# Kernel optimization log

Hardware: AMD Instinct MI355X
Metric: run time of the kernel (lower is better)

The kernel has to match this reference:

```python
import jax, jax.numpy as jnp
import numpy as np

D = 128      # embedding_dim
E = 50000    # positive edges per metapath
S = 16       # negative samples per edge
N_A = 100000 # nodes of type A (head type of both metapaths)
N_B = 50000  # nodes of type B (tail type of metapath 1)


def setup_inputs() -> dict:
    key = jax.random.key(0)
    ks = jax.random.split(key, 10)
    emb_A = jax.random.normal(ks[0], (N_A, D), dtype=jnp.float32)
    emb_B = jax.random.normal(ks[1], (N_B, D), dtype=jnp.float32)
    # nn.init.uniform_(a=-1, b=1)
    rel_emb = jax.random.uniform(ks[2], (2, D, D), dtype=jnp.float32, minval=-1.0, maxval=1.0)
    edge_index_m0 = jax.random.randint(ks[3], (2, E), 0, N_A)  # A -> A
    edge_index_m1 = jnp.stack([
        jax.random.randint(ks[4], (E,), 0, N_A),               # heads: type A
        jax.random.randint(ks[5], (E,), 0, N_B),               # tails: type B
    ])
    neg_head_m0 = jax.random.randint(ks[6], (E, S), 0, N_A)
    neg_head_m1 = jax.random.randint(ks[7], (E, S), 0, N_A)
    neg_tail_m0 = jax.random.randint(ks[8], (E, S), 0, N_A)
    neg_tail_m1 = jax.random.randint(ks[9], (E, S), 0, N_B)
    return dict(emb_A=emb_A, emb_B=emb_B, rel_emb=rel_emb,
                edge_index_m0=edge_index_m0, edge_index_m1=edge_index_m1,
                neg_head_m0=neg_head_m0, neg_head_m1=neg_head_m1,
                neg_tail_m0=neg_tail_m0, neg_tail_m1=neg_tail_m1)


# The torch module computes score = (A K B^T).sum(dim=1); summing the [E,E]
# score matrix over dim 1 equals contracting with sum_j b_j, so we never
# materialize the [E,E] (or [E*S, E*S]) matrix -- same math, fused reduction.

def _pos_score(K, emb_h, emb_t, edge_index):
    s = emb_t[edge_index[1]].sum(0)          # [d] = sum_j b_j
    return emb_h[edge_index[0]] @ (K @ s)    # [E]


def _neg_head_score(K, emb_h, neg):
    # predict(mode='head'): emb_A = emb_h[neg.reshape(-1)],
    # idx_B = edge_index[0][arange(E)*S] == neg[:, 0],
    # side_B = (K @ emb_h[idx_B].T).repeat_interleave(S, -1); sum over columns
    # == K @ (S * sum_j emb_h[neg[j, 0]]).
    s = neg.shape[1]
    c = K @ (s * emb_h[neg[:, 0]].sum(0))    # [d]
    return emb_h[neg.reshape(-1)] @ c        # [E*S]


def _neg_tail_score(K, emb_t, neg):
    # predict(mode='tail'): emb_B = emb_t[neg.reshape(-1)],
    # idx_A = edge_index[1][arange(E)*S] == neg[:, 0],
    # side_A = (emb_t[idx_A] @ K).repeat_interleave(S, 0); row sums of
    # side_A @ emb_B^T == side_A @ sum_j emb_B[j].
    s = neg.shape[1]
    sb = emb_t[neg.reshape(-1)].sum(0)       # [d]
    base = (emb_t[neg[:, 0]] @ K) @ sb       # [E]
    return jnp.repeat(base, s)               # [E*S]


def reference(emb_A, emb_B, rel_emb, edge_index_m0, edge_index_m1,
              neg_head_m0, neg_head_m1, neg_tail_m0, neg_tail_m1):
    K0, K1 = rel_emb[0], rel_emb[1]
    pos0 = _pos_score(K0, emb_A, emb_A, edge_index_m0)   # [E]
    pos1 = _pos_score(K1, emb_A, emb_B, edge_index_m1)   # [E]
    nh0 = _neg_head_score(K0, emb_A, neg_head_m0)        # [E*S]
    nh1 = _neg_head_score(K1, emb_A, neg_head_m1)        # [E*S]
    nt0 = _neg_tail_score(K0, emb_A, neg_tail_m0)        # [E*S]
    nt1 = _neg_tail_score(K1, emb_B, neg_tail_m1)        # [E*S]
    return jnp.concatenate([pos0, pos1, nh0, nh1, nt0, nt1])
```

## Files before the change

kernel.cpp:

```cpp
#include <hip/hip_runtime.h>
#include <stdint.h>

#define D 128
#define E_EDGES 50000
#define S_NEG 16
#define N_A 100000
#define N_B 50000
#define ES (E_EDGES * S_NEG)

#define HW 12500
#define ACH 38
#define BCH 34

#define GA1 500
#define GB1 250
#define NCPY 16
#define GA2 391
#define GB2 196

__device__ inline float dot4(float4 a, float4 b) {
    return a.x * b.x + a.y * b.y + a.z * b.z + a.w * b.w;
}
__device__ inline void fma16(float* acc, const float4 w, const float4 x) {
    acc[0]  += w.x * x.x; acc[1]  += w.x * x.y; acc[2]  += w.x * x.z; acc[3]  += w.x * x.w;
    acc[4]  += w.y * x.x; acc[5]  += w.y * x.y; acc[6]  += w.y * x.z; acc[7]  += w.y * x.w;
    acc[8]  += w.z * x.x; acc[9]  += w.z * x.y; acc[10] += w.z * x.z; acc[11] += w.z * x.w;
    acc[12] += w.w * x.x; acc[13] += w.w * x.y; acc[14] += w.w * x.z; acc[15] += w.w * x.w;
}
__device__ inline void fma8(float* acc, const float2 w, const float4 x) {
    acc[0] += w.x * x.x; acc[1] += w.x * x.y; acc[2] += w.x * x.z; acc[3] += w.x * x.w;
    acc[4] += w.y * x.x; acc[5] += w.y * x.y; acc[6] += w.y * x.z; acc[7] += w.y * x.w;
}


__global__ void k_hist(const int* __restrict__ ei0, const int* __restrict__ ei1,
                       const int* __restrict__ nh0, const int* __restrict__ nh1,
                       const int* __restrict__ nt0, const int* __restrict__ nt1,
                       uint32_t* __restrict__ partA, uint32_t* __restrict__ partB,
                       float* __restrict__ svec) {
    __shared__ uint32_t h[HW];
    const int tid = threadIdx.x;
    if (blockIdx.x == 0) {
        for (int i = tid; i < NCPY * 6 * D; i += 512) svec[i] = 0.f;
    }
    for (int w = tid; w < HW; w += 512) h[w] = 0;
    __syncthreads();

    const int b = blockIdx.x;
    if (b < 2 * ACH) {
        const int c = b >> 1, hh = b & 1;
        const unsigned lo = hh * 50000u;
        uint32_t* dst = partA + (size_t)b * HW;
        if (c >= 2 && c < 6) {
            const int* src = (c < 4) ? nh0 : nh1;
            const long long base = (long long)(c & 1) * 25000 * S_NEG;
            for (int i = tid; i < 25000; i += 512) {
                const unsigned r = (unsigned)src[base + (long long)i * S_NEG] - lo;
                if (r < 50000u) atomicAdd(&h[r >> 2], 1u << ((r & 3u) * 8u));
            }
        } else {
            const int* srcp = (c < 2) ? (ei0 + E_EDGES + c * 25000)
                                      : (nt0 + (c - 6) * 25000);
            const int4* src4 = reinterpret_cast<const int4*>(srcp);
            for (int i = tid; i < 6250; i += 512) {
                const int4 v = src4[i];
                unsigned r;
                r = (unsigned)v.x - lo; if (r < 50000u) atomicAdd(&h[r >> 2], 1u << ((r & 3u) * 8u));
                r = (unsigned)v.y - lo; if (r < 50000u) atomicAdd(&h[r >> 2], 1u << ((r & 3u) * 8u));
                r = (unsigned)v.z - lo; if (r < 50000u) atomicAdd(&h[r >> 2], 1u << ((r & 3u) * 8u));
                r = (unsigned)v.w - lo; if (r < 50000u) atomicAdd(&h[r >> 2], 1u << ((r & 3u) * 8u));
            }
        }
        __syncthreads();
        for (int w = tid; w < HW; w += 512) dst[w] = h[w];
    } else {
        const int c = b - 2 * ACH;
        uint32_t* dst = partB + (size_t)c * HW;
        const int* srcp = (c < 2) ? (ei1 + E_EDGES + c * 25000)
                                  : (nt1 + (c - 2) * 25000);
        const int4* src4 = reinterpret_cast<const int4*>(srcp);
        for (int i = tid; i < 6250; i += 512) {
            const int4 v = src4[i];
            unsigned r;
            r = (unsigned)v.x; if (r < 50000u) atomicAdd(&h[r >> 2], 1u << ((r & 3u) * 8u));
            r = (unsigned)v.y; if (r < 50000u) atomicAdd(&h[r >> 2], 1u << ((r & 3u) * 8u));
            r = (unsigned)v.z; if (r < 50000u) atomicAdd(&h[r >> 2], 1u << ((r & 3u) * 8u));
            r = (unsigned)v.w; if (r < 50000u) atomicAdd(&h[r >> 2], 1u << ((r & 3u) * 8u));
        }
        __syncthreads();
        for (int w = tid; w < HW; w += 512) dst[w] = h[w];
    }
}

__global__ void __launch_bounds__(256, 4)
k_scan1(const float* __restrict__ embA, const float* __restrict__ embB,
        const uint32_t* __restrict__ partA, const uint32_t* __restrict__ partB,
        float* __restrict__ svec) {
    __shared__ float sds[4 * 512];
    __shared__ float4 cwbuf[200];
    const int tid = threadIdx.x;
    const int l = tid & 31;
    const int grp = tid >> 5;
    const int wid = tid >> 6;
    float* svdst = svec + (size_t)(blockIdx.x & (NCPY - 1)) * (6 * D);

    if ((int)blockIdx.x < GA1) {
        const int nb = blockIdx.x * 200;
        if (tid < 200) {
            const int n = nb + tid;
            const int hh = (n >= 50000);
            const int sh = (n & 3) * 8;
            const uint32_t* p = partA + (size_t)hh * HW + ((n - hh * 50000) >> 2);
            unsigned s0 = 0, s1 = 0, s2 = 0, s3 = 0;
#pragma unroll
            for (int c = 0; c < 2; ++c)  s0 += (p[(size_t)(c * 2) * HW] >> sh) & 255u;
#pragma unroll
            for (int c = 2; c < 4; ++c)  s1 += (p[(size_t)(c * 2) * HW] >> sh) & 255u;
#pragma unroll
            for (int c = 4; c < 6; ++c)  s2 += (p[(size_t)(c * 2) * HW] >> sh) & 255u;
#pragma unroll 8
            for (int c = 6; c < 38; ++c) s3 += (p[(size_t)(c * 2) * HW] >> sh) & 255u;
            cwbuf[tid] = make_float4((float)s0, (float)s1, (float)s2, (float)s3);
        }
        __syncthreads();

        const int r0 = nb + grp * 25;
        const int lr0 = grp * 25;
        const float* base = embA + 4 * l;
        float acc[16];
#pragma unroll
        for (int k = 0; k < 16; ++k) acc[k] = 0.f;
        float4 wc[5], xc[5];
#pragma unroll
        for (int u = 0; u < 5; ++u) {
            wc[u] = cwbuf[lr0 + u];
            xc[u] = *reinterpret_cast<const float4*>(base + (size_t)(r0 + u) * D);
        }
#pragma unroll
        for (int b = 0; b < 5; ++b) {
            float4 wn[5], xn[5];
            if (b < 4) {
#pragma unroll
                for (int u = 0; u < 5; ++u) {
                    const int rr = (b + 1) * 5 + u;
                    wn[u] = cwbuf[lr0 + rr];
                    xn[u] = *reinterpret_cast<const float4*>(base + (size_t)(r0 + rr) * D);
                }
            }
#pragma unroll
            for (int u = 0; u < 5; ++u) fma16(acc, wc[u], xc[u]);
            if (b < 4) {
#pragma unroll
                for (int u = 0; u < 5; ++u) { wc[u] = wn[u]; xc[u] = xn[u]; }
            }
        }
#pragma unroll
        for (int k = 0; k < 16; ++k) acc[k] += __shfl_xor(acc[k], 32);
        if ((tid & 32) == 0) {
            float* w0 = sds + wid * 512;
#pragma unroll
            for (int p = 0; p < 4; ++p)
                *reinterpret_cast<float4*>(w0 + p * 128 + 4 * l) =
                    make_float4(acc[4 * p], acc[4 * p + 1], acc[4 * p + 2], acc[4 * p + 3]);
        }
        __syncthreads();
        for (int j = tid; j < 512; j += 256)
            atomicAdd(&svdst[j], sds[j] + sds[512 + j] + sds[1024 + j] + sds[1536 + j]);
    } else {
        const int nb = (blockIdx.x - GA1) * 200;
        if (tid < 200) {
            const int n = nb + tid;
            const int sh = (n & 3) * 8;
            const uint32_t* p = partB + (n >> 2);
            unsigned s0 = 0, s1 = 0;
#pragma unroll
            for (int c = 0; c < 2; ++c)  s0 += (p[(size_t)c * HW] >> sh) & 255u;
#pragma unroll 8
            for (int c = 2; c < 34; ++c) s1 += (p[(size_t)c * HW] >> sh) & 255u;
            reinterpret_cast<float2*>(cwbuf)[tid] = make_float2((float)s0, (float)s1);
        }
        __syncthreads();
        const float2* cw2 = reinterpret_cast<const float2*>(cwbuf);

        const int r0 = nb + grp * 25;
        const int lr0 = grp * 25;
        const float* base = embB + 4 * l;
        float acc[8];
#pragma unroll
        for (int k = 0; k < 8; ++k) acc[k] = 0.f;
        float2 wc[5]; float4 xc[5];
#pragma unroll
        for (int u = 0; u < 5; ++u) {
            wc[u] = cw2[lr0 + u];
            xc[u] = *reinterpret_cast<const float4*>(base + (size_t)(r0 + u) * D);
        }
#pragma unroll
        for (int b = 0; b < 5; ++b) {
            float2 wn[5]; float4 xn[5];
            if (b < 4) {
#pragma unroll
                for (int u = 0; u < 5; ++u) {
                    const int rr = (b + 1) * 5 + u;
                    wn[u] = cw2[lr0 + rr];
                    xn[u] = *reinterpret_cast<const float4*>(base + (size_t)(r0 + rr) * D);
                }
            }
#pragma unroll
            for (int u = 0; u < 5; ++u) fma8(acc, wc[u], xc[u]);
            if (b < 4) {
#pragma unroll
                for (int u = 0; u < 5; ++u) { wc[u] = wn[u]; xc[u] = xn[u]; }
            }
        }
#pragma unroll
        for (int k = 0; k < 8; ++k) acc[k] += __shfl_xor(acc[k], 32);
        if ((tid & 32) == 0) {
            float* w0 = sds + wid * 256;
#pragma unroll
            for (int p = 0; p < 2; ++p)
                *reinterpret_cast<float4*>(w0 + p * 128 + 4 * l) =
                    make_float4(acc[4 * p], acc[4 * p + 1], acc[4 * p + 2], acc[4 * p + 3]);
        }
        __syncthreads();
        for (int j = tid; j < 256; j += 256)
            atomicAdd(&svdst[512 + j], sds[j] + sds[256 + j] + sds[512 + j] + sds[768 + j]);
    }
}

__global__ void __launch_bounds__(256, 4)
k_scan2(const float* __restrict__ embA, const float* __restrict__ embB,
        const float* __restrict__ rel, const float* __restrict__ svec,
        float* __restrict__ PA, float* __restrict__ PB) {
    __shared__ float sv[6 * D];
    __shared__ float sc[6 * D];
    const int tid = threadIdx.x;

    for (int e = tid; e < 6 * D; e += 256) {
        float s = 0.f;
#pragma unroll
        for (int c = 0; c < NCPY; ++c) s += svec[c * (6 * D) + e];
        sv[e] = s;
    }
    __syncthreads();

    for (int e = tid; e < 6 * D; e += 256) {
        const int j = e >> 7, i = e & 127;
        const int plane = (j == 0) ? 0 : (j == 1) ? 4 : (j == 5) ? 5 : (j - 1);
        const float4* Kp4 = reinterpret_cast<const float4*>(
            rel + (size_t)(j & 1) * (D * D) + (size_t)i * D);
        const float* s = sv + plane * D;
        float acc = 0.f;
#pragma unroll
        for (int k = 0; k < 32; ++k) {
            const float4 kk = Kp4[k];
            acc += kk.x * s[4 * k] + kk.y * s[4 * k + 1]
                 + kk.z * s[4 * k + 2] + kk.w * s[4 * k + 3];
        }
        sc[e] = acc * ((j == 2 || j == 3) ? (float)S_NEG : 1.0f);
    }
    __syncthreads();

    if ((int)blockIdx.x < GA2) {
        const int n = blockIdx.x * 256 + tid;
        const int nc = min(n, N_A - 1);
        const float4* row = reinterpret_cast<const float4*>(embA + (size_t)nc * D);
        float a0 = 0.f, a1 = 0.f, a2 = 0.f, a3 = 0.f, a4 = 0.f;
#pragma unroll 8
        for (int k = 0; k < 32; ++k) {
            const float4 x = row[k];
            a0 += dot4(x, *reinterpret_cast<const float4*>(sc + 0 * D + 4 * k));
            a1 += dot4(x, *reinterpret_cast<const float4*>(sc + 1 * D + 4 * k));
            a2 += dot4(x, *reinterpret_cast<const float4*>(sc + 2 * D + 4 * k));
            a3 += dot4(x, *reinterpret_cast<const float4*>(sc + 3 * D + 4 * k));
            a4 += dot4(x, *reinterpret_cast<const float4*>(sc + 4 * D + 4 * k));
        }
        if (n < N_A) {
            PA[0 * (size_t)N_A + n] = a0;
            PA[1 * (size_t)N_A + n] = a1;
            PA[2 * (size_t)N_A + n] = a2;
            PA[3 * (size_t)N_A + n] = a3;
            PA[4 * (size_t)N_A + n] = a4;
        }
    } else {
        const int n = (blockIdx.x - GA2) * 256 + tid;
        const int nc = min(n, N_B - 1);
        const float4* row = reinterpret_cast<const float4*>(embB + (size_t)nc * D);
        float a0 = 0.f;
#pragma unroll 8
        for (int k = 0; k < 32; ++k) {
            const float4 x = row[k];
            a0 += dot4(x, *reinterpret_cast<const float4*>(sc + 5 * D + 4 * k));
        }
        if (n < N_B) PB[n] = a0;
    }
}

__global__ void k_scatter(const int* __restrict__ ei0, const int* __restrict__ ei1,
                          const int* __restrict__ nh0, const int* __restrict__ nh1,
                          const int* __restrict__ nt0, const int* __restrict__ nt1,
                          const float* __restrict__ PA, const float* __restrict__ PB,
                          float* __restrict__ out) {
    const int total4 = (2 * E_EDGES + 4 * ES) / 4;
    const float* P0 = PA;
    const float* P1 = PA + (size_t)N_A;
    const float* P2 = PA + (size_t)2 * N_A;
    const float* P3 = PA + (size_t)3 * N_A;
    const float* P4 = PA + (size_t)4 * N_A;
    for (int t = blockIdx.x * blockDim.x + threadIdx.x; t < total4;
         t += gridDim.x * blockDim.x) {
        const int e = t * 4;
        float4 v;
        if (e < E_EDGES) {
            const int4 i4 = *reinterpret_cast<const int4*>(ei0 + e);
            v = make_float4(P0[i4.x], P0[i4.y], P0[i4.z], P0[i4.w]);
        } else if (e < 2 * E_EDGES) {
            const int4 i4 = *reinterpret_cast<const int4*>(ei1 + (e - E_EDGES));
            v = make_float4(P1[i4.x], P1[i4.y], P1[i4.z], P1[i4.w]);
        } else if (e < 2 * E_EDGES + ES) {
            const int4 i4 = *reinterpret_cast<const int4*>(nh0 + (e - 2 * E_EDGES));
            v = make_float4(P2[i4.x], P2[i4.y], P2[i4.z], P2[i4.w]);
        } else if (e < 2 * E_EDGES + 2 * ES) {
            const int4 i4 = *reinterpret_cast<const int4*>(nh1 + (e - 2 * E_EDGES - ES));
            v = make_float4(P3[i4.x], P3[i4.y], P3[i4.z], P3[i4.w]);
        } else if (e < 2 * E_EDGES + 3 * ES) {
            const int i = e - 2 * E_EDGES - 2 * ES;
            const float s = P4[nt0[(i >> 4) << 4]];
            v = make_float4(s, s, s, s);
        } else {
            const int i = e - 2 * E_EDGES - 3 * ES;
            const float s = PB[nt1[(i >> 4) << 4]];
            v = make_float4(s, s, s, s);
        }
        *reinterpret_cast<float4*>(out + e) = v;
    }
}

extern "C" void kernel_launch(void* const* d_in, const int* in_sizes, int n_in,
                              void* d_out, int out_size, void* d_ws, size_t ws_size,
                              hipStream_t stream) {
    const float* embA = (const float*)d_in[0];
    const float* embB = (const float*)d_in[1];
    const float* rel  = (const float*)d_in[2];
    const int* ei0 = (const int*)d_in[3];
    const int* ei1 = (const int*)d_in[4];
    const int* nh0 = (const int*)d_in[5];
    const int* nh1 = (const int*)d_in[6];
    const int* nt0 = (const int*)d_in[7];
    const int* nt1 = (const int*)d_in[8];
    float* out = (float*)d_out;

    uint32_t* partA = (uint32_t*)d_ws;
    uint32_t* partB = partA + (size_t)2 * ACH * HW;
    float* svec = (float*)(partB + (size_t)BCH * HW);
    float* PA   = svec + (size_t)NCPY * 6 * D;
    float* PB   = PA + (size_t)5 * N_A;

    k_hist<<<2 * ACH + BCH, 512, 0, stream>>>(ei0, ei1, nh0, nh1, nt0, nt1,
                                              partA, partB, svec);
    k_scan1<<<GA1 + GB1, 256, 0, stream>>>(embA, embB, partA, partB, svec);
    k_scan2<<<GA2 + GB2, 256, 0, stream>>>(embA, embB, rel, svec, PA, PB);
    k_scatter<<<2048, 256, 0, stream>>>(ei0, ei1, nh0, nh1, nt0, nt1, PA, PB, out);
}
```

Baseline: 220.5 us.

## Compute K·s vectors once in last scan1 block and coalesce scan2 row dots

The per-block recomputation of the six K·s vectors (a 128x128 matvec per plane) moves out of every scan2 block. The last-finishing scan1 block, found with an atomic done counter and threadfence, now computes them once into a global cvec. scan2 is restructured so 16 threads cooperate on each embedding row with coalesced float4 loads and shuffle reductions, instead of one thread striding a whole row. This adds a completion counter and a serial tail on one block of scan1, and raises the scan2 block count.

```diff
diff --git a/kernel.cpp b/kernel.cpp
--- a/kernel.cpp
+++ b/kernel.cpp
@@ -15,8 +15,10 @@
 #define GA1 500
 #define GB1 250
 #define NCPY 16
-#define GA2 391
-#define GB2 196
+
+#define S2_ROWS 128
+#define GA2 ((N_A + S2_ROWS - 1) / S2_ROWS)
+#define GB2 ((N_B + S2_ROWS - 1) / S2_ROWS)
 
 __device__ inline float dot4(float4 a, float4 b) {
     return a.x * b.x + a.y * b.y + a.z * b.z + a.w * b.w;
@@ -37,11 +39,12 @@
                        const int* __restrict__ nh0, const int* __restrict__ nh1,
                        const int* __restrict__ nt0, const int* __restrict__ nt1,
                        uint32_t* __restrict__ partA, uint32_t* __restrict__ partB,
-                       float* __restrict__ svec) {
+                       float* __restrict__ svec, unsigned* __restrict__ done) {
     __shared__ uint32_t h[HW];
     const int tid = threadIdx.x;
     if (blockIdx.x == 0) {
         for (int i = tid; i < NCPY * 6 * D; i += 512) svec[i] = 0.f;
+        if (tid == 0) *done = 0u;
     }
     for (int w = tid; w < HW; w += 512) h[w] = 0;
     __syncthreads();
@@ -94,10 +97,14 @@
 
 __global__ void __launch_bounds__(256, 4)
 k_scan1(const float* __restrict__ embA, const float* __restrict__ embB,
+        const float* __restrict__ rel,
         const uint32_t* __restrict__ partA, const uint32_t* __restrict__ partB,
-        float* __restrict__ svec) {
+        float* __restrict__ svec, float* __restrict__ cvec,
+        unsigned* __restrict__ done) {
     __shared__ float sds[4 * 512];
     __shared__ float4 cwbuf[200];
+    __shared__ float sv[6 * D];
+    __shared__ int lastflag;
     const int tid = threadIdx.x;
     const int l = tid & 31;
     const int grp = tid >> 5;
@@ -225,73 +232,98 @@
         for (int j = tid; j < 256; j += 256)
             atomicAdd(&svdst[512 + j], sds[j] + sds[256 + j] + sds[512 + j] + sds[768 + j]);
     }
-}
-
-__global__ void __launch_bounds__(256, 4)
-k_scan2(const float* __restrict__ embA, const float* __restrict__ embB,
-        const float* __restrict__ rel, const float* __restrict__ svec,
-        float* __restrict__ PA, float* __restrict__ PB) {
-    __shared__ float sv[6 * D];
-    __shared__ float sc[6 * D];
+
+    __threadfence();
+    if (tid == 0)
+        lastflag = (atomicAdd(done, 1u) == (unsigned)(GA1 + GB1 - 1)) ? 1 : 0;
+    __syncthreads();
+    if (lastflag) {
+        for (int e = tid; e < 6 * D; e += 256) {
+            float s = 0.f;
+#pragma unroll
+            for (int c = 0; c < NCPY; ++c)
+                s += __hip_atomic_load(&svec[c * (6 * D) + e],
+                                       __ATOMIC_RELAXED, __HIP_MEMORY_SCOPE_AGENT);
+            sv[e] = s;
+        }
+        __syncthreads();
+        for (int e = tid; e < 6 * D; e += 256) {
+            const int j = e >> 7, i = e & 127;
+            const int plane = (j == 0) ? 0 : (j == 1) ? 4 : (j == 5) ? 5 : (j - 1);
+            const float4* Kp4 = reinterpret_cast<const float4*>(
+                rel + (size_t)(j & 1) * (D * D) + (size_t)i * D);
+            const float* s = sv + plane * D;
+            float acc = 0.f;
+#pragma unroll
+            for (int k = 0; k < 32; ++k) {
+                const float4 kk = Kp4[k];
+                acc += kk.x * s[4 * k] + kk.y * s[4 * k + 1]
+                     + kk.z * s[4 * k + 2] + kk.w * s[4 * k + 3];
+            }
+            cvec[j * D + i] = acc * ((j == 2 || j == 3) ? (float)S_NEG : 1.0f);
+        }
+    }
+}
+
+__global__ void k_scan2(const float* __restrict__ embA, const float* __restrict__ embB,
+                        const float* __restrict__ cvec,
+                        float* __restrict__ PA, float* __restrict__ PB) {
     const int tid = threadIdx.x;
-
-    for (int e = tid; e < 6 * D; e += 256) {
-        float s = 0.f;
-#pragma unroll
-        for (int c = 0; c < NCPY; ++c) s += svec[c * (6 * D) + e];
-        sv[e] = s;
-    }
-    __syncthreads();
-
-    for (int e = tid; e < 6 * D; e += 256) {
-        const int j = e >> 7, i = e & 127;
-        const int plane = (j == 0) ? 0 : (j == 1) ? 4 : (j == 5) ? 5 : (j - 1);
-        const float4* Kp4 = reinterpret_cast<const float4*>(
-            rel + (size_t)(j & 1) * (D * D) + (size_t)i * D);
-        const float* s = sv + plane * D;
-        float acc = 0.f;
-#pragma unroll
-        for (int k = 0; k < 32; ++k) {
-            const float4 kk = Kp4[k];
-            acc += kk.x * s[4 * k] + kk.y * s[4 * k + 1]
-                 + kk.z * s[4 * k + 2] + kk.w * s[4 * k + 3];
-        }
-        sc[e] = acc * ((j == 2 || j == 3) ? (float)S_NEG : 1.0f);
-    }
-    __syncthreads();
+    const int sub = tid & 15;
+    const int rloc = tid >> 4;
 
     if ((int)blockIdx.x < GA2) {
-        const int n = blockIdx.x * 256 + tid;
-        const int nc = min(n, N_A - 1);
-        const float4* row = reinterpret_cast<const float4*>(embA + (size_t)nc * D);
-        float a0 = 0.f, a1 = 0.f, a2 = 0.f, a3 = 0.f, a4 = 0.f;
-#pragma unroll 8
-        for (int k = 0; k < 32; ++k) {
-            const float4 x = row[k];
-            a0 += dot4(x, *reinterpret_cast<const float4*>(sc + 0 * D + 4 * k));
-            a1 += dot4(x, *reinterpret_cast<const float4*>(sc + 1 * D + 4 * k));
-            a2 += dot4(x, *reinterpret_cast<const float4*>(sc + 2 * D + 4 * k));
-            a3 += dot4(x, *reinterpret_cast<const float4*>(sc + 3 * D + 4 * k));
-            a4 += dot4(x, *reinterpret_cast<const float4*>(sc + 4 * D + 4 * k));
-        }
-        if (n < N_A) {
-            PA[0 * (size_t)N_A + n] = a0;
-            PA[1 * (size_t)N_A + n] = a1;
-            PA[2 * (size_t)N_A + n] = a2;
-            PA[3 * (size_t)N_A + n] = a3;
-            PA[4 * (size_t)N_A + n] = a4;
+        float4 c0[5], c1[5];
+#pragma unroll
+        for (int j = 0; j < 5; ++j) {
+            c0[j] = *reinterpret_cast<const float4*>(cvec + j * D + sub * 8);
+            c1[j] = *reinterpret_cast<const float4*>(cvec + j * D + sub * 8 + 4);
+        }
+        const int base = blockIdx.x * S2_ROWS;
+#pragma unroll 2
+        for (int it = 0; it < S2_ROWS / 16; ++it) {
+            const int row = base + it * 16 + rloc;
+            const int rc = min(row, N_A - 1);
+            const float* rp = embA + (size_t)rc * D + sub * 8;
+            const float4 x0 = *reinterpret_cast<const float4*>(rp);
+            const float4 x1 = *reinterpret_cast<const float4*>(rp + 4);
+            float p0 = dot4(x0, c0[0]) + dot4(x1, c1[0]);
+            float p1 = dot4(x0, c0[1]) + dot4(x1, c1[1]);
+            float p2 = dot4(x0, c0[2]) + dot4(x1, c1[2]);
+            float p3 = dot4(x0, c0[3]) + dot4(x1, c1[3]);
+            float p4 = dot4(x0, c0[4]) + dot4(x1, c1[4]);
+#pragma unroll
+            for (int m = 1; m < 16; m <<= 1) {
+                p0 += __shfl_xor(p0, m);
+                p1 += __shfl_xor(p1, m);
+                p2 += __shfl_xor(p2, m);
+                p3 += __shfl_xor(p3, m);
+                p4 += __shfl_xor(p4, m);
+            }
+            if (row < N_A) {
+                if (sub == 0)      PA[row] = p0;
+                else if (sub == 1) PA[(size_t)N_A + row] = p1;
+                else if (sub == 2) PA[(size_t)2 * N_A + row] = p2;
+                else if (sub == 3) PA[(size_t)3 * N_A + row] = p3;
+                else if (sub == 4) PA[(size_t)4 * N_A + row] = p4;
+            }
         }
     } else {
-        const int n = (blockIdx.x - GA2) * 256 + tid;
-        const int nc = min(n, N_B - 1);
-        const float4* row = reinterpret_cast<const float4*>(embB + (size_t)nc * D);
-        float a0 = 0.f;
-#pragma unroll 8
-        for (int k = 0; k < 32; ++k) {
-            const float4 x = row[k];
-            a0 += dot4(x, *reinterpret_cast<const float4*>(sc + 5 * D + 4 * k));
-        }
-        if (n < N_B) PB[n] = a0;
+        const float4 c0 = *reinterpret_cast<const float4*>(cvec + 5 * D + sub * 8);
+        const float4 c1 = *reinterpret_cast<const float4*>(cvec + 5 * D + sub * 8 + 4);
+        const int base = (blockIdx.x - GA2) * S2_ROWS;
+#pragma unroll 2
+        for (int it = 0; it < S2_ROWS / 16; ++it) {
+            const int row = base + it * 16 + rloc;
+            const int rc = min(row, N_B - 1);
+            const float* rp = embB + (size_t)rc * D + sub * 8;
+            const float4 x0 = *reinterpret_cast<const float4*>(rp);
+            const float4 x1 = *reinterpret_cast<const float4*>(rp + 4);
+            float p = dot4(x0, c0) + dot4(x1, c1);
+#pragma unroll
+            for (int m = 1; m < 16; m <<= 1) p += __shfl_xor(p, m);
+            if (row < N_B && sub == 0) PB[row] = p;
+        }
     }
 }
 
@@ -352,12 +384,15 @@
     uint32_t* partA = (uint32_t*)d_ws;
     uint32_t* partB = partA + (size_t)2 * ACH * HW;
     float* svec = (float*)(partB + (size_t)BCH * HW);
-    float* PA   = svec + (size_t)NCPY * 6 * D;
+    unsigned* done = (unsigned*)(svec + (size_t)NCPY * 6 * D);
+    float* cvec = (float*)(done + 4);
+    float* PA   = cvec + 6 * D;
     float* PB   = PA + (size_t)5 * N_A;
 
     k_hist<<<2 * ACH + BCH, 512, 0, stream>>>(ei0, ei1, nh0, nh1, nt0, nt1,
-                                              partA, partB, svec);
-    k_scan1<<<GA1 + GB1, 256, 0, stream>>>(embA, embB, partA, partB, svec);
-    k_scan2<<<GA2 + GB2, 256, 0, stream>>>(embA, embB, rel, svec, PA, PB);
+                                              partA, partB, svec, done);
+    k_scan1<<<GA1 + GB1, 256, 0, stream>>>(embA, embB, rel, partA, partB,
+                                           svec, cvec, done);
+    k_scan2<<<GA2 + GB2, 256, 0, stream>>>(embA, embB, cvec, PA, PB);
     k_scatter<<<2048, 256, 0, stream>>>(ei0, ei1, nh0, nh1, nt0, nt1, PA, PB, out);
 }
```

Measured after the change: 281.8 us. +27.8%, slower.
